# Optimization experiments

Hardware: AMD Instinct MI355X
Metric: run time of the kernel (lower is better)

Reference implementation:

```python
import jax, jax.numpy as jnp
import numpy as np

N_MLP = 16
LATENT = 1024
S0, S1, S2, OUT = 512, 256, 128, 3


def _make_grid(n_grid_step):
    # matches np.meshgrid (indexing='xy') then reshape(-1): points (x, y)
    p = np.linspace(-1.0, 1.0, n_grid_step, dtype=np.float32)
    X, Y = np.meshgrid(p, p)
    return jnp.asarray(np.stack([X.ravel(), Y.ravel()], axis=-1))  # [G, 2]


def setup_inputs() -> dict:
    key = jax.random.key(0)
    ks = jax.random.split(key, 12)
    sc = lambda fan_in: 1.0 / np.sqrt(fan_in)
    inp = {
        "x0": jax.random.normal(ks[0], (LATENT,), jnp.float32),
        "W0a": jax.random.normal(ks[1], (N_MLP, S0, LATENT), jnp.float32) * sc(LATENT),
        "b0a": jax.random.normal(ks[2], (N_MLP, S0), jnp.float32) * sc(LATENT),
        "W0b": jax.random.normal(ks[3], (N_MLP, S0, 2), jnp.float32) * sc(2),
        "b0b": jax.random.normal(ks[4], (N_MLP, S0), jnp.float32) * sc(2),
        "W1": jax.random.normal(ks[5], (N_MLP, S1, S0), jnp.float32) * sc(S0),
        "b1": jax.random.normal(ks[6], (N_MLP, S1), jnp.float32) * sc(S0),
        "W2": jax.random.normal(ks[7], (N_MLP, S2, S1), jnp.float32) * sc(S1),
        "b2": jax.random.normal(ks[8], (N_MLP, S2), jnp.float32) * sc(S1),
        "W3": jax.random.normal(ks[9], (N_MLP, OUT, S2), jnp.float32) * sc(S2),
        "b3": jax.random.normal(ks[10], (N_MLP, OUT), jnp.float32) * sc(S2),
        "n_grid_step": 128,
    }
    return inp


def reference(x0, W0a, b0a, W0b, b0b, W1, b1, W2, b2, W3, b3, n_grid_step):
    grid = _make_grid(n_grid_step)  # [G, 2], constant (requires_grad=False)
    # latent branch: [m, S0]
    y0_a = jnp.einsum('mol,l->mo', W0a, x0) + b0a
    # grid branch: [m, G, S0]
    y0_b = jnp.einsum('moi,gi->mgo', W0b, grid) + b0b[:, None, :]
    h = jax.nn.relu(y0_a[:, None, :] + y0_b)                        # [m,G,S0]
    h = jax.nn.relu(jnp.einsum('moh,mgh->mgo', W1, h) + b1[:, None, :])  # [m,G,S1]
    h = jax.nn.relu(jnp.einsum('moh,mgh->mgo', W2, h) + b2[:, None, :])  # [m,G,S2]
    out = jnp.tanh(jnp.einsum('moh,mgh->mgo', W3, h) + b3[:, None, :])   # [m,G,3]
    return out.reshape(-1, OUT)  # [m*G, 3]
```

## Files before the change

### kernel.cpp

```cpp
#include <hip/hip_runtime.h>
#include <hip/hip_bf16.h>
#include <cstdint>

typedef __bf16 bf16_t;
typedef bf16_t bf16x8 __attribute__((ext_vector_type(8)));
typedef bf16_t bf16x4 __attribute__((ext_vector_type(4)));
typedef float  f32x4  __attribute__((ext_vector_type(4)));

#define S0 512
#define S1 256
#define S2 128
#define NGRID 128
#define GPTS (NGRID*NGRID)

#define WS_BASE  0u
#define WS_W1P   32768u
#define WS_W2P   4227072u
#define WS_W3P   5275648u
#define WS_BASEC 5341184u
#define WS_WXYC  5373952u
#define WS_IDX   5439488u
#define WS_LIN   5472256u
#define WS_F     5505024u
#define WS_CNT   5570560u

__device__ __forceinline__ float tanh_fast(float x) {
  float e = __builtin_amdgcn_exp2f(x * 2.88539008f);
  return fmaf(-2.0f, __builtin_amdgcn_rcpf(e + 1.0f), 1.0f);
}

__device__ __forceinline__ bf16x8 ld_h1(const bf16_t* s, int row, int colk) {
  const int byte = row*512 + (((colk*2) ^ ((row & 7) << 4)));
  return *(const bf16x8*)((const char*)s + byte);
}
__device__ __forceinline__ void st_h1(bf16_t* s, int row, int col, bf16x4 v) {
  const int byte = row*512 + (((col*2) ^ ((row & 7) << 4)));
  *(bf16x4*)((char*)s + byte) = v;
}

__global__ __launch_bounds__(256) void prep_a(
    const float* __restrict__ x0, const float* __restrict__ W0a,
    const float* __restrict__ b0a, const float* __restrict__ b0b,
    const float* __restrict__ W2, const float* __restrict__ W3,
    float* __restrict__ base, bf16_t* __restrict__ W2p, bf16_t* __restrict__ W3p)
{
  if (blockIdx.x < 2048) {
    int wid = (blockIdx.x << 2) + (threadIdx.x >> 6);
    int L = threadIdx.x & 63;
    int m = wid >> 9, o = wid & 511;
    const float* wrow = W0a + ((size_t)(m*S0 + o) << 10);
    float acc = 0.f;
#pragma unroll
    for (int i = 0; i < 4; ++i) {
      f32x4 wv = *(const f32x4*)(wrow + i*256 + L*4);
      f32x4 xv = *(const f32x4*)(x0   + i*256 + L*4);
      acc += wv.x*xv.x + wv.y*xv.y + wv.z*xv.z + wv.w*xv.w;
    }
#pragma unroll
    for (int s = 32; s; s >>= 1) acc += __shfl_xor(acc, s, 64);
    if (L == 0) base[m*S0 + o] = acc + b0a[m*S0 + o] + b0b[m*S0 + o];
    return;
  }

  int T = (blockIdx.x - 2048) * 256 + threadIdx.x;
  const float* src = nullptr;
  bf16_t* dst = nullptr;
  if (T < 65536) {
    int L = T & 63, nt = (T >> 6) & 7, ks = (T >> 9) & 7, m = T >> 12;
    int n = nt*16 + (L & 15), k0 = ks*32 + ((L >> 4) & 3)*8;
    src = W2 + (size_t)(m*S2 + n)*S1 + k0;
    dst = W2p + (size_t)T*8;
  } else {
    int T3 = T - 65536;
    int L = T3 & 63, ks = (T3 >> 6) & 3, m = T3 >> 8;
    int n = L & 15, k0 = ks*32 + ((L >> 4) & 3)*8;
    dst = W3p + (size_t)T3*8;
    if (n < 3) src = W3 + (size_t)(m*3 + n)*S2 + k0;
  }
  bf16x8 v;
  if (src) {
    f32x4 a = *(const f32x4*)src;
    f32x4 b = *(const f32x4*)(src + 4);
    v[0]=(bf16_t)a.x; v[1]=(bf16_t)a.y; v[2]=(bf16_t)a.z; v[3]=(bf16_t)a.w;
    v[4]=(bf16_t)b.x; v[5]=(bf16_t)b.y; v[6]=(bf16_t)b.z; v[7]=(bf16_t)b.w;
  } else {
#pragma unroll
    for (int j = 0; j < 8; ++j) v[j] = (bf16_t)0.f;
  }
  *(bf16x8*)dst = v;
}

__global__ __launch_bounds__(256) void classify_k(
    const float* __restrict__ base, const float* __restrict__ W0b,
    float* __restrict__ basec, float* __restrict__ wxyc,
    int* __restrict__ idx, int* __restrict__ lin,
    int* __restrict__ Kc, int* __restrict__ nlin, float* __restrict__ F)
{
  __shared__ int sc[512];
  const int m = blockIdx.x, t = threadIdx.x;
  float b[2], wx[2], wy[2]; int fa[2], fl[2];
#pragma unroll
  for (int h = 0; h < 2; ++h) {
    const int k = t + h*256;
    b[h]  = base[m*S0 + k];
    wx[h] = W0b[(m*S0 + k)*2];
    wy[h] = W0b[(m*S0 + k)*2 + 1];
    const float aw = fabsf(wx[h]) + fabsf(wy[h]);
    const int dead = (b[h] + aw) <= 0.f;
    fl[h] = (!dead) && ((b[h] - aw) >= 0.f);
    fa[h] = (!dead) && (!fl[h]);
    sc[k] = fa[h] | (fl[h] << 16);
  }
  __syncthreads();
  for (int off = 1; off < 512; off <<= 1) {
    int v0 = sc[t], v1 = sc[t+256];
    int u0 = (t >= off) ? sc[t-off] : 0;
    int u1 = (t+256 >= off) ? sc[t+256-off] : 0;
    __syncthreads();
    sc[t] = v0 + u0; sc[t+256] = v1 + u1;
    __syncthreads();
  }
  const int tot = sc[511];
  const int KcM = tot & 0xffff, nlM = tot >> 16;
#pragma unroll
  for (int h = 0; h < 2; ++h) {
    const int k = t + h*256;
    const int incl = sc[k];
    if (fa[h]) {
      const int p = (incl & 0xffff) - 1;
      idx[m*S0 + p] = k;
      basec[m*S0 + p] = b[h];
      wxyc[m*S0*2 + 2*p]     = wx[h];
      wxyc[m*S0*2 + 2*p + 1] = wy[h];
    } else if (fl[h]) {
      lin[m*S0 + ((incl >> 16) - 1)] = k;
    }
  }
  for (int s = t; s < 512; s += 256) {
    if (s >= KcM) {
      idx[m*S0 + s] = 0;
      basec[m*S0 + s] = 0.f;
      wxyc[m*S0*2 + 2*s] = 0.f;
      wxyc[m*S0*2 + 2*s + 1] = 0.f;
    }
  }
  for (int i = t; i < 1024; i += 256) F[m*1024 + i] = 0.f;
  if (t == 0) { Kc[m] = KcM; nlin[m] = nlM; }
}

__global__ __launch_bounds__(256) void prep_b(
    const float* __restrict__ W1, const float* __restrict__ base,
    const float* __restrict__ W0b,
    const int* __restrict__ idx, const int* __restrict__ lin,
    const int* __restrict__ Kc, const int* __restrict__ nlin,
    bf16_t* __restrict__ W1p, float* __restrict__ F)
{
  if (blockIdx.x < 1024) {
    const int T = blockIdx.x*256 + threadIdx.x;
    const int L = T & 63, nt = (T >> 6) & 15, ks = (T >> 10) & 15, m = T >> 14;
    const int KcM = Kc[m];
    const int n = nt*16 + (L & 15), kb = ks*32 + ((L >> 4) & 3)*8;
    const float* wrow = W1 + (size_t)(m*S1 + n)*S0;
    const int* ip = idx + m*S0 + kb;
    bf16x8 v;
#pragma unroll
    for (int j = 0; j < 8; ++j)
      v[j] = (kb + j < KcM) ? (bf16_t)wrow[ip[j]] : (bf16_t)0.f;
    *(bf16x8*)(W1p + (size_t)T*8) = v;
  } else {
    const int b2 = blockIdx.x - 1024;
    const int m = b2 >> 4, s = b2 & 15, n = threadIdx.x;
    const int nl = nlin[m];
    float a0 = 0.f, ax = 0.f, ay = 0.f;
    const float* wrow = W1 + (size_t)(m*S1 + n)*S0;
    for (int j = s; j < nl; j += 16) {
      const int k = lin[m*S0 + j];
      const float w = wrow[k];
      a0 = fmaf(w, base[m*S0 + k], a0);
      ax = fmaf(w, W0b[(m*S0 + k)*2], ax);
      ay = fmaf(w, W0b[(m*S0 + k)*2 + 1], ay);
    }
    float* fp = F + ((size_t)m*S1 + n)*4;
    atomicAdd(fp + 0, a0);
    atomicAdd(fp + 1, ax);
    atomicAdd(fp + 2, ay);
  }
}

template<int NKS>
__device__ __forceinline__ void l1_compute(
    const bf16_t* __restrict__ bp1, const float* __restrict__ bc,
    const float* __restrict__ wc, bf16_t* sStg,
    const int w, const int L, const int quad,
    const float yv, const float xg0, const float xg1, f32x4 (&acc1)[8][4])
{
  bf16x8 Bc[4];
#pragma unroll
  for (int n = 0; n < 4; ++n) Bc[n] = *(const bf16x8*)(bp1 + (size_t)n*512);

#pragma unroll 2
  for (int ks = 0; ks < NKS; ++ks) {
    const bf16_t* bpk = bp1 + (size_t)ks*8192;
    bf16x8 Bn[4];
    if (ks + 1 < NKS) {
#pragma unroll
      for (int n = 0; n < 4; ++n)
        Bn[n] = *(const bf16x8*)(bpk + 8192 + (size_t)n*512);
    }

    const int kk = ks*32 + quad*8;
    f32x4 cA  = *(const f32x4*)(bc + kk);
    f32x4 cB  = *(const f32x4*)(bc + kk + 4);
    f32x4 wv0 = *(const f32x4*)(wc + kk*2);
    f32x4 wv1 = *(const f32x4*)(wc + kk*2 + 4);
    f32x4 wv2 = *(const f32x4*)(wc + kk*2 + 8);
    f32x4 wv3 = *(const f32x4*)(wc + kk*2 + 12);

    float t[8], wx[8];
    t[0] = fmaf(wv0.y, yv, cA.x); wx[0] = wv0.x;
    t[1] = fmaf(wv0.w, yv, cA.y); wx[1] = wv0.z;
    t[2] = fmaf(wv1.y, yv, cA.z); wx[2] = wv1.x;
    t[3] = fmaf(wv1.w, yv, cA.w); wx[3] = wv1.z;
    t[4] = fmaf(wv2.y, yv, cB.x); wx[4] = wv2.x;
    t[5] = fmaf(wv2.w, yv, cB.y); wx[5] = wv2.z;
    t[6] = fmaf(wv3.y, yv, cB.z); wx[6] = wv3.x;
    t[7] = fmaf(wv3.w, yv, cB.w); wx[7] = wv3.z;

    bf16x8 g0, g1;
#pragma unroll
    for (int j = 0; j < 8; ++j) {
      g0[j] = (bf16_t)fmaxf(fmaf(wx[j], xg0, t[j]), 0.f);
      g1[j] = (bf16_t)fmaxf(fmaf(wx[j], xg1, t[j]), 0.f);
    }

    bf16_t* stg = sStg + (ks & 1)*4096;
    *(bf16x8*)(stg + (((2*w  ) << 6) + L)*8) = g0;
    *(bf16x8*)(stg + (((2*w+1) << 6) + L)*8) = g1;
    asm volatile("s_waitcnt lgkmcnt(0)" ::: "memory");
    __builtin_amdgcn_s_barrier();
    __builtin_amdgcn_sched_barrier(0);

#pragma unroll
    for (int mt = 0; mt < 8; ++mt) {
      bf16x8 af = *(const bf16x8*)(stg + ((mt << 6) + L)*8);
#pragma unroll
      for (int n = 0; n < 4; ++n)
        acc1[mt][n] = __builtin_amdgcn_mfma_f32_16x16x32_bf16(Bc[n], af, acc1[mt][n], 0, 0, 0);
    }
    if (ks + 1 < NKS) {
#pragma unroll
      for (int n = 0; n < 4; ++n) Bc[n] = Bn[n];
    }
  }
}

__global__ __launch_bounds__(256, 2) void fused_mlp_k(
    const float* __restrict__ basec, const float* __restrict__ wxyc,
    const float* __restrict__ F, const int* __restrict__ Kc,
    const bf16_t* __restrict__ W1p, const bf16_t* __restrict__ W2p,
    const bf16_t* __restrict__ W3p,
    const float* __restrict__ b1, const float* __restrict__ b2,
    const float* __restrict__ b3, float* __restrict__ out)
{
  __shared__ __align__(16) bf16_t sLDS[128*256];

  const int bid = blockIdx.x;
  const int m   = bid >> 7;
  const int st  = bid & 127;

  const int tid  = threadIdx.x;
  const int w    = tid >> 6, L = tid & 63;
  const int quad = L >> 4, lrow = L & 15;

  const float step = 2.0f / 127.0f;
  const float yv  = -1.0f + (float)st * step;
  const float xv0 = -1.0f + (float)lrow * step;
  const float xg0 = xv0 + (float)((2*w  )*16)*step;
  const float xg1 = xv0 + (float)((2*w+1)*16)*step;

  const float* bc = basec + m*S0;
  const float* wc = wxyc + m*(S0*2);
  const int nks = (Kc[m] + 31) >> 5;

  f32x4 zero = {0.f, 0.f, 0.f, 0.f};
  f32x4 acc1[8][4];
#pragma unroll
  for (int a = 0; a < 8; ++a)
#pragma unroll
    for (int b = 0; b < 4; ++b) acc1[a][b] = zero;

  const bf16_t* bp1 = W1p + (((size_t)(m*16)*16 + w*4)*64 + L)*8;
#define L1_CASE(NN) case NN: l1_compute<NN>(bp1, bc, wc, sLDS, w, L, quad, yv, xg0, xg1, acc1); break;
  switch (nks) {
    L1_CASE(16) L1_CASE(15) L1_CASE(14) L1_CASE(13)
    L1_CASE(12) L1_CASE(11) L1_CASE(10) L1_CASE(9)
    L1_CASE(8)  L1_CASE(7)  L1_CASE(6)  L1_CASE(5)
    L1_CASE(4)  L1_CASE(3)  L1_CASE(2)  L1_CASE(1)
    default: break;
  }
#undef L1_CASE
  __syncthreads();

#pragma unroll
  for (int nb = 0; nb < 4; ++nb) {
    const int col = w*64 + nb*16 + quad*4;
    f32x4 bb = *(const f32x4*)(b1 + m*S1 + col);
    float cterm[4], fx[4];
#pragma unroll
    for (int p = 0; p < 4; ++p) {
      f32x4 Fv = *(const f32x4*)(F + ((size_t)m*S1 + col + p)*4);
      cterm[p] = fmaf(Fv.z, yv, bb[p] + Fv.x);
      fx[p] = Fv.y;
    }
#pragma unroll
    for (int mt = 0; mt < 8; ++mt) {
      const int row = mt*16 + lrow;
      const float xr = xv0 + (float)(mt*16)*step;
      bf16x4 v;
#pragma unroll
      for (int p = 0; p < 4; ++p)
        v[p] = (bf16_t)fmaxf(acc1[mt][nb][p] + fmaf(fx[p], xr, cterm[p]), 0.f);
      st_h1(sLDS, row, col, v);
    }
  }
  __syncthreads();

  f32x4 acc2[8][2];
#pragma unroll
  for (int a = 0; a < 8; ++a) { acc2[a][0] = zero; acc2[a][1] = zero; }
  const bf16_t* bp2 = W2p + (((size_t)(m*8)*8 + w*2)*64 + L)*8;
#pragma unroll 2
  for (int ks = 0; ks < 8; ++ks) {
    const int k2 = ks*32 + quad*8;
    bf16x8 b0f = *(const bf16x8*)(bp2 + (size_t)ks*4096);
    bf16x8 b1f = *(const bf16x8*)(bp2 + (size_t)ks*4096 + 512);
#pragma unroll
    for (int mt = 0; mt < 8; ++mt) {
      bf16x8 af = ld_h1(sLDS, mt*16 + lrow, k2);
      acc2[mt][0] = __builtin_amdgcn_mfma_f32_16x16x32_bf16(b0f, af, acc2[mt][0], 0, 0, 0);
      acc2[mt][1] = __builtin_amdgcn_mfma_f32_16x16x32_bf16(b1f, af, acc2[mt][1], 0, 0, 0);
    }
  }
  __syncthreads();

  bf16_t* sH2 = sLDS;
#pragma unroll
  for (int nb = 0; nb < 2; ++nb) {
    const int col = w*32 + nb*16 + quad*4;
    f32x4 bb = *(const f32x4*)(b2 + m*S2 + col);
#pragma unroll
    for (int mt = 0; mt < 8; ++mt) {
      const int row = mt*16 + lrow;
      bf16x4 v;
#pragma unroll
      for (int p = 0; p < 4; ++p)
        v[p] = (bf16_t)fmaxf(acc2[mt][nb][p] + bb[p], 0.f);
      *(bf16x4*)(&sH2[row*136 + col]) = v;
    }
  }
  __syncthreads();

  f32x4 acc3[2] = {zero, zero};
#pragma unroll
  for (int ks = 0; ks < 4; ++ks) {
    bf16x8 bfr = *(const bf16x8*)(W3p + (((size_t)m*4 + ks)*64 + L)*8);
    bf16x8 af0 = *(const bf16x8*)(&sH2[((w  )*16 + lrow)*136 + ks*32 + quad*8]);
    bf16x8 af1 = *(const bf16x8*)(&sH2[((w+4)*16 + lrow)*136 + ks*32 + quad*8]);
    acc3[0] = __builtin_amdgcn_mfma_f32_16x16x32_bf16(bfr, af0, acc3[0], 0, 0, 0);
    acc3[1] = __builtin_amdgcn_mfma_f32_16x16x32_bf16(bfr, af1, acc3[1], 0, 0, 0);
  }
  if (quad == 0) {
#pragma unroll
    for (int ri = 0; ri < 2; ++ri) {
      const int rb = w + ri*4;
      const size_t o = ((size_t)m*GPTS + (size_t)st*128 + rb*16 + lrow)*3;
      out[o + 0] = tanh_fast(acc3[ri][0] + b3[m*3 + 0]);
      out[o + 1] = tanh_fast(acc3[ri][1] + b3[m*3 + 1]);
      out[o + 2] = tanh_fast(acc3[ri][2] + b3[m*3 + 2]);
    }
  }
}

extern "C" void kernel_launch(void* const* d_in, const int* in_sizes, int n_in,
                              void* d_out, int out_size, void* d_ws, size_t ws_size,
                              hipStream_t stream) {
  const float* x0  = (const float*)d_in[0];
  const float* W0a = (const float*)d_in[1];
  const float* b0a = (const float*)d_in[2];
  const float* W0b = (const float*)d_in[3];
  const float* b0b = (const float*)d_in[4];
  const float* W1  = (const float*)d_in[5];
  const float* b1  = (const float*)d_in[6];
  const float* W2  = (const float*)d_in[7];
  const float* b2  = (const float*)d_in[8];
  const float* W3  = (const float*)d_in[9];
  const float* b3  = (const float*)d_in[10];

  char* ws = (char*)d_ws;
  float*  base  = (float*)(ws + WS_BASE);
  bf16_t* W1p   = (bf16_t*)(ws + WS_W1P);
  bf16_t* W2p   = (bf16_t*)(ws + WS_W2P);
  bf16_t* W3p   = (bf16_t*)(ws + WS_W3P);
  float*  basec = (float*)(ws + WS_BASEC);
  float*  wxyc  = (float*)(ws + WS_WXYC);
  int*    idx   = (int*)(ws + WS_IDX);
  int*    lin   = (int*)(ws + WS_LIN);
  float*  F     = (float*)(ws + WS_F);
  int*    Kc    = (int*)(ws + WS_CNT);
  int*    nlin  = (int*)(ws + WS_CNT + 64);
  float*  out   = (float*)d_out;

  prep_a<<<2368, 256, 0, stream>>>(x0, W0a, b0a, b0b, W2, W3, base, W2p, W3p);
  classify_k<<<16, 256, 0, stream>>>(base, W0b, basec, wxyc, idx, lin, Kc, nlin, F);
  prep_b<<<1280, 256, 0, stream>>>(W1, base, W0b, idx, lin, Kc, nlin, W1p, F);
  fused_mlp_k<<<2048, 256, 0, stream>>>(basec, wxyc, F, Kc, W1p, W2p, W3p, b1, b2, b3, out);
}
```

Baseline: 197.0 us.

## Software-pipeline layer-1 activation generation ahead of MFMA with double-buffered LDS

The layer-1 loop now generates and stores the relu'd input tile for step ks+1 into the other LDS buffer while step ks's tile is consumed by MFMAs. This leaves one barrier per iteration, placed after the MFMAs instead of between generation and use. The A-fragment loads are split into two halves so MFMAs on the first half can run while the second half loads. This is meant to hide generation ALU work and LDS latency behind matrix ops, at the cost of more live registers and more reliance on careful barrier placement.

```diff
diff --git a/kernel.cpp b/kernel.cpp
--- a/kernel.cpp
+++ b/kernel.cpp
@@ -194,20 +194,7 @@
     const int w, const int L, const int quad,
     const float yv, const float xg0, const float xg1, f32x4 (&acc1)[8][4])
 {
-  bf16x8 Bc[4];
-#pragma unroll
-  for (int n = 0; n < 4; ++n) Bc[n] = *(const bf16x8*)(bp1 + (size_t)n*512);
-
-#pragma unroll 2
-  for (int ks = 0; ks < NKS; ++ks) {
-    const bf16_t* bpk = bp1 + (size_t)ks*8192;
-    bf16x8 Bn[4];
-    if (ks + 1 < NKS) {
-#pragma unroll
-      for (int n = 0; n < 4; ++n)
-        Bn[n] = *(const bf16x8*)(bpk + 8192 + (size_t)n*512);
-    }
-
+  auto GEN = [&](int ks) {
     const int kk = ks*32 + quad*8;
     f32x4 cA  = *(const f32x4*)(bc + kk);
     f32x4 cB  = *(const f32x4*)(bc + kk + 4);
@@ -215,7 +202,6 @@
     f32x4 wv1 = *(const f32x4*)(wc + kk*2 + 4);
     f32x4 wv2 = *(const f32x4*)(wc + kk*2 + 8);
     f32x4 wv3 = *(const f32x4*)(wc + kk*2 + 12);
-
     float t[8], wx[8];
     t[0] = fmaf(wv0.y, yv, cA.x); wx[0] = wv0.x;
     t[1] = fmaf(wv0.w, yv, cA.y); wx[1] = wv0.z;
@@ -225,32 +211,60 @@
     t[5] = fmaf(wv2.w, yv, cB.y); wx[5] = wv2.z;
     t[6] = fmaf(wv3.y, yv, cB.z); wx[6] = wv3.x;
     t[7] = fmaf(wv3.w, yv, cB.w); wx[7] = wv3.z;
-
     bf16x8 g0, g1;
 #pragma unroll
     for (int j = 0; j < 8; ++j) {
       g0[j] = (bf16_t)fmaxf(fmaf(wx[j], xg0, t[j]), 0.f);
       g1[j] = (bf16_t)fmaxf(fmaf(wx[j], xg1, t[j]), 0.f);
     }
-
     bf16_t* stg = sStg + (ks & 1)*4096;
     *(bf16x8*)(stg + (((2*w  ) << 6) + L)*8) = g0;
     *(bf16x8*)(stg + (((2*w+1) << 6) + L)*8) = g1;
+  };
+
+  bf16x8 Bc[4], Bn[4];
+#pragma unroll
+  for (int n = 0; n < 4; ++n) Bc[n] = *(const bf16x8*)(bp1 + (size_t)n*512);
+  GEN(0);
+  asm volatile("s_waitcnt lgkmcnt(0)" ::: "memory");
+  asm volatile("s_barrier" ::: "memory");
+  __builtin_amdgcn_sched_barrier(0);
+
+#pragma unroll 2
+  for (int ks = 0; ks < NKS; ++ks) {
+    const bf16_t* stg = sStg + (ks & 1)*4096;
+    bf16x8 af0[4];
+#pragma unroll
+    for (int mt = 0; mt < 4; ++mt)
+      af0[mt] = *(const bf16x8*)(stg + ((mt << 6) + L)*8);
+    if (ks + 1 < NKS) {
+#pragma unroll
+      for (int n = 0; n < 4; ++n)
+        Bn[n] = *(const bf16x8*)(bp1 + (size_t)(ks+1)*8192 + (size_t)n*512);
+      GEN(ks + 1);
+    }
     asm volatile("s_waitcnt lgkmcnt(0)" ::: "memory");
-    __builtin_amdgcn_s_barrier();
     __builtin_amdgcn_sched_barrier(0);
-
-#pragma unroll
-    for (int mt = 0; mt < 8; ++mt) {
-      bf16x8 af = *(const bf16x8*)(stg + ((mt << 6) + L)*8);
+#pragma unroll
+    for (int mt = 0; mt < 4; ++mt)
 #pragma unroll
       for (int n = 0; n < 4; ++n)
-        acc1[mt][n] = __builtin_amdgcn_mfma_f32_16x16x32_bf16(Bc[n], af, acc1[mt][n], 0, 0, 0);
-    }
-    if (ks + 1 < NKS) {
-#pragma unroll
-      for (int n = 0; n < 4; ++n) Bc[n] = Bn[n];
-    }
+        acc1[mt][n] = __builtin_amdgcn_mfma_f32_16x16x32_bf16(Bc[n], af0[mt], acc1[mt][n], 0, 0, 0);
+    bf16x8 af1[4];
+#pragma unroll
+    for (int mt = 0; mt < 4; ++mt)
+      af1[mt] = *(const bf16x8*)(stg + (((mt + 4) << 6) + L)*8);
+    asm volatile("s_waitcnt lgkmcnt(0)" ::: "memory");
+    __builtin_amdgcn_sched_barrier(0);
+#pragma unroll
+    for (int mt = 0; mt < 4; ++mt)
+#pragma unroll
+      for (int n = 0; n < 4; ++n)
+        acc1[mt+4][n] = __builtin_amdgcn_mfma_f32_16x16x32_bf16(Bc[n], af1[mt], acc1[mt+4][n], 0, 0, 0);
+    asm volatile("s_barrier" ::: "memory");
+    __builtin_amdgcn_sched_barrier(0);
+#pragma unroll
+    for (int n = 0; n < 4; ++n) Bc[n] = Bn[n];
   }
 }
 
```

Measured after the change: 194.3 us. No clear change (-1.4%).

## Repartition layer-1 MFMA work to remove per-k-step LDS staging and barriers

Applied to the files above, without the earlier changes.

Layer 1 now splits the 128x256 output tile so each wave owns 64 rows by 128 columns, rather than all 128 rows by 64 columns. Each wave computes the ReLU'd first-layer activations for its own rows in registers and feeds them straight into the MFMAs. This removes the per-k-step LDS staging writes, the s_barrier and the LDS reads of the A fragments, as well as the barrier before the epilogue. In exchange, each wave loads twice as many W1 B-fragments per k-step (8 instead of 4, plus 8 prefetched), and the activation math is done for 4 row groups instead of 2. That raises register pressure and global-load traffic, with launch bounds of 256 threads and 2 blocks.

```diff
diff --git a/kernel.cpp b/kernel.cpp
--- a/kernel.cpp
+++ b/kernel.cpp
@@ -190,24 +190,21 @@
 template<int NKS>
 __device__ __forceinline__ void l1_compute(
     const bf16_t* __restrict__ bp1, const float* __restrict__ bc,
-    const float* __restrict__ wc, bf16_t* sStg,
-    const int w, const int L, const int quad,
-    const float yv, const float xg0, const float xg1, f32x4 (&acc1)[8][4])
+    const float* __restrict__ wc, const int quad,
+    const float yv, const float xr0, const float step16,
+    f32x4 (&acc1)[4][8])
 {
-  bf16x8 Bc[4];
-#pragma unroll
-  for (int n = 0; n < 4; ++n) Bc[n] = *(const bf16x8*)(bp1 + (size_t)n*512);
+  bf16x8 Bc[8], Bn[8];
+#pragma unroll
+  for (int n = 0; n < 8; ++n) Bc[n] = *(const bf16x8*)(bp1 + (size_t)n*512);
 
 #pragma unroll 2
   for (int ks = 0; ks < NKS; ++ks) {
-    const bf16_t* bpk = bp1 + (size_t)ks*8192;
-    bf16x8 Bn[4];
     if (ks + 1 < NKS) {
 #pragma unroll
-      for (int n = 0; n < 4; ++n)
-        Bn[n] = *(const bf16x8*)(bpk + 8192 + (size_t)n*512);
-    }
-
+      for (int n = 0; n < 8; ++n)
+        Bn[n] = *(const bf16x8*)(bp1 + (size_t)(ks+1)*8192 + (size_t)n*512);
+    }
     const int kk = ks*32 + quad*8;
     f32x4 cA  = *(const f32x4*)(bc + kk);
     f32x4 cB  = *(const f32x4*)(bc + kk + 4);
@@ -226,30 +223,20 @@
     t[6] = fmaf(wv3.y, yv, cB.z); wx[6] = wv3.x;
     t[7] = fmaf(wv3.w, yv, cB.w); wx[7] = wv3.z;
 
-    bf16x8 g0, g1;
-#pragma unroll
-    for (int j = 0; j < 8; ++j) {
-      g0[j] = (bf16_t)fmaxf(fmaf(wx[j], xg0, t[j]), 0.f);
-      g1[j] = (bf16_t)fmaxf(fmaf(wx[j], xg1, t[j]), 0.f);
-    }
-
-    bf16_t* stg = sStg + (ks & 1)*4096;
-    *(bf16x8*)(stg + (((2*w  ) << 6) + L)*8) = g0;
-    *(bf16x8*)(stg + (((2*w+1) << 6) + L)*8) = g1;
-    asm volatile("s_waitcnt lgkmcnt(0)" ::: "memory");
-    __builtin_amdgcn_s_barrier();
-    __builtin_amdgcn_sched_barrier(0);
-
-#pragma unroll
-    for (int mt = 0; mt < 8; ++mt) {
-      bf16x8 af = *(const bf16x8*)(stg + ((mt << 6) + L)*8);
-#pragma unroll
-      for (int n = 0; n < 4; ++n)
-        acc1[mt][n] = __builtin_amdgcn_mfma_f32_16x16x32_bf16(Bc[n], af, acc1[mt][n], 0, 0, 0);
+#pragma unroll
+    for (int i = 0; i < 4; ++i) {
+      const float xr = xr0 + (float)i * step16;
+      bf16x8 af;
+#pragma unroll
+      for (int j = 0; j < 8; ++j)
+        af[j] = (bf16_t)fmaxf(fmaf(wx[j], xr, t[j]), 0.f);
+#pragma unroll
+      for (int n = 0; n < 8; ++n)
+        acc1[i][n] = __builtin_amdgcn_mfma_f32_16x16x32_bf16(Bc[n], af, acc1[i][n], 0, 0, 0);
     }
     if (ks + 1 < NKS) {
 #pragma unroll
-      for (int n = 0; n < 4; ++n) Bc[n] = Bn[n];
+      for (int n = 0; n < 8; ++n) Bc[n] = Bn[n];
     }
   }
 }
@@ -271,26 +258,28 @@
   const int tid  = threadIdx.x;
   const int w    = tid >> 6, L = tid & 63;
   const int quad = L >> 4, lrow = L & 15;
+  const int rh   = w >> 1;
+  const int ch   = w & 1;
 
   const float step = 2.0f / 127.0f;
   const float yv  = -1.0f + (float)st * step;
   const float xv0 = -1.0f + (float)lrow * step;
-  const float xg0 = xv0 + (float)((2*w  )*16)*step;
-  const float xg1 = xv0 + (float)((2*w+1)*16)*step;
+  const float xr0 = xv0 + (float)(rh*64)*step;
+  const float step16 = 16.0f*step;
 
   const float* bc = basec + m*S0;
   const float* wc = wxyc + m*(S0*2);
   const int nks = (Kc[m] + 31) >> 5;
 
   f32x4 zero = {0.f, 0.f, 0.f, 0.f};
-  f32x4 acc1[8][4];
-#pragma unroll
-  for (int a = 0; a < 8; ++a)
-#pragma unroll
-    for (int b = 0; b < 4; ++b) acc1[a][b] = zero;
-
-  const bf16_t* bp1 = W1p + (((size_t)(m*16)*16 + w*4)*64 + L)*8;
-#define L1_CASE(NN) case NN: l1_compute<NN>(bp1, bc, wc, sLDS, w, L, quad, yv, xg0, xg1, acc1); break;
+  f32x4 acc1[4][8];
+#pragma unroll
+  for (int a = 0; a < 4; ++a)
+#pragma unroll
+    for (int b = 0; b < 8; ++b) acc1[a][b] = zero;
+
+  const bf16_t* bp1 = W1p + (((size_t)(m*16)*16 + ch*8)*64 + L)*8;
+#define L1_CASE(NN) case NN: l1_compute<NN>(bp1, bc, wc, quad, yv, xr0, step16, acc1); break;
   switch (nks) {
     L1_CASE(16) L1_CASE(15) L1_CASE(14) L1_CASE(13)
     L1_CASE(12) L1_CASE(11) L1_CASE(10) L1_CASE(9)
@@ -299,11 +288,10 @@
     default: break;
   }
 #undef L1_CASE
-  __syncthreads();
-
-#pragma unroll
-  for (int nb = 0; nb < 4; ++nb) {
-    const int col = w*64 + nb*16 + quad*4;
+
+#pragma unroll
+  for (int nb = 0; nb < 8; ++nb) {
+    const int col = ch*128 + nb*16 + quad*4;
     f32x4 bb = *(const f32x4*)(b1 + m*S1 + col);
     float cterm[4], fx[4];
 #pragma unroll
@@ -313,13 +301,14 @@
       fx[p] = Fv.y;
     }
 #pragma unroll
-    for (int mt = 0; mt < 8; ++mt) {
-      const int row = mt*16 + lrow;
-      const float xr = xv0 + (float)(mt*16)*step;
+    for (int i = 0; i < 4; ++i) {
+      const int rb  = rh*4 + i;
+      const int row = rb*16 + lrow;
+      const float xr = xv0 + (float)(rb*16)*step;
       bf16x4 v;
 #pragma unroll
       for (int p = 0; p < 4; ++p)
-        v[p] = (bf16_t)fmaxf(acc1[mt][nb][p] + fmaf(fx[p], xr, cterm[p]), 0.f);
+        v[p] = (bf16_t)fmaxf(acc1[i][nb][p] + fmaf(fx[p], xr, cterm[p]), 0.f);
       st_h1(sLDS, row, col, v);
     }
   }
```

After: 196.3 us. About the same (-0.4%).
